# Performance work log

Hardware: AMD Instinct MI355X
Metric: run time of the kernel (lower is better)

## Reference

```python
import jax, jax.numpy as jnp
import numpy as np

B, SEQ, C, H, L = 2, 512, 768, 12, 6
OBS = ACT = GOAL = 64
MAXEP = 1000
D = C // H
T3 = 3 * SEQ  # stacked (z, state, action) tokens per timestep


def _ln(x, g, b):
    m = jnp.mean(x, -1, keepdims=True)
    v = jnp.mean((x - m) ** 2, -1, keepdims=True)
    return (x - m) * jax.lax.rsqrt(v + 1e-5) * g + b


def setup_inputs() -> dict:
    key = jax.random.key(0)
    it = iter(jax.random.split(key, 64))
    nrm = lambda shape, s=0.02: jax.random.normal(next(it), shape, jnp.float32) * s
    z = lambda *s: jnp.zeros(s, jnp.float32)
    o = lambda *s: jnp.ones(s, jnp.float32)
    return dict(
        states=jax.random.normal(next(it), (B, SEQ, OBS), jnp.float32),
        actions=jax.random.normal(next(it), (B, SEQ, ACT), jnp.float32),
        goals=jax.random.normal(next(it), (B, 1, GOAL), jnp.float32),
        traj_mask=jnp.ones((B, SEQ), bool),
        timesteps=jax.random.randint(next(it), (B, SEQ), 0, MAXEP),
        W_s=nrm((OBS, C)), b_s=z(C),
        W_a=nrm((ACT, C)), b_a=z(C),
        W_g=nrm((GOAL, C)), b_g=z(C),
        E_t=nrm((MAXEP, C)),
        ln0_g=o(C), ln0_b=z(C),
        Wq=nrm((L, C, C)), bq=z(L, C),
        Wk=nrm((L, C, C)), bk=z(L, C),
        Wv=nrm((L, C, C)), bv=z(L, C),
        Wp=nrm((L, C, C)), bp=z(L, C),
        ln1_g=o(L, C), ln1_b=z(L, C),
        W1=nrm((L, C, 4 * C)), b1=z(L, 4 * C),
        W2=nrm((L, 4 * C, C)), b2=z(L, C),
        ln2_g=o(L, C), ln2_b=z(L, C),
        W_ps=nrm((C, OBS)), b_ps=z(OBS),
        W_pa=nrm((C, ACT)), b_pa=z(ACT),
    )


def _forward(states, actions, goals, timesteps,
             W_s, b_s, W_a, b_a, W_g, b_g, E_t, ln0_g, ln0_b,
             Wq, bq, Wk, bk, Wv, bv, Wp, bp, ln1_g, ln1_b,
             W1, b1, W2, b2, ln2_g, ln2_b, W_ps, b_ps, W_pa, b_pa):
    te = E_t[timesteps]  # [B,SEQ,C] time embeddings (use_pe_as_timestep path)
    s_emb = states @ W_s + b_s + te
    a_emb = actions @ W_a + b_a + te
    g = jnp.broadcast_to(goals, (goals.shape[0], SEQ, goals.shape[2]))
    z_emb = g @ W_g + b_g + te  # GOAL_CONDITION path
    # interleave (z, s, a) per timestep -> [B, 3*SEQ, C]
    x = jnp.stack((z_emb, s_emb, a_emb), axis=2).reshape(states.shape[0], T3, C)
    x = _ln(x, ln0_g, ln0_b)
    mask = jnp.tril(jnp.ones((T3, T3), bool))
    scale = 1.0 / np.sqrt(D)
    for l in range(L):
        q = (x @ Wq[l] + bq[l]).reshape(-1, T3, H, D)
        k = (x @ Wk[l] + bk[l]).reshape(-1, T3, H, D)
        v = (x @ Wv[l] + bv[l]).reshape(-1, T3, H, D)
        sc = jnp.einsum('bqhd,bkhd->bhqk', q, k) * scale
        sc = jnp.where(mask, sc, -jnp.inf)
        w = jax.nn.softmax(sc, axis=-1)
        att = jnp.einsum('bhqk,bkhd->bqhd', w, v).reshape(-1, T3, C)
        x = x + att @ Wp[l] + bp[l]
        x = _ln(x, ln1_g[l], ln1_b[l])
        h = jax.nn.gelu(x @ W1[l] + b1[l], approximate=False)
        x = x + h @ W2[l] + b2[l]
        x = _ln(x, ln2_g[l], ln2_b[l])
    x = x.reshape(-1, SEQ, 3, C)
    state_preds = x[:, :, 2] @ W_ps + b_ps     # read off action-token positions
    action_preds = jnp.tanh(x[:, :, 1] @ W_pa + b_pa)  # state-token positions
    return jnp.stack((state_preds, action_preds))  # [2,B,SEQ,64]


def reference(states, actions, goals, traj_mask, timesteps,
              W_s, b_s, W_a, b_a, W_g, b_g, E_t, ln0_g, ln0_b,
              Wq, bq, Wk, bk, Wv, bv, Wp, bp, ln1_g, ln1_b,
              W1, b1, W2, b2, ln2_g, ln2_b, W_ps, b_ps, W_pa, b_pa):
    del traj_mask  # unused on the GOAL_CONDITION path
    return _forward(states, actions, goals, timesteps,
                    W_s, b_s, W_a, b_a, W_g, b_g, E_t, ln0_g, ln0_b,
                    Wq, bq, Wk, bk, Wv, bv, Wp, bp, ln1_g, ln1_b,
                    W1, b1, W2, b2, ln2_g, ln2_b, W_ps, b_ps, W_pa, b_pa)
```

## Files before the change

### kernel.cpp

```cpp
#include <hip/hip_runtime.h>

#define SEQ 512
#define T3 1536
#define CDIM 768
#define NH 12
#define HD 64
#define NL 6

typedef __attribute__((ext_vector_type(8))) short bh8;
typedef __attribute__((ext_vector_type(4))) short s4;
typedef __attribute__((ext_vector_type(4))) float f4;

__device__ inline short f2bf(float f) {
    union { float f; unsigned u; } x; x.f = f;
    unsigned r = x.u + 0x7FFFu + ((x.u >> 16) & 1u);
    return (short)(r >> 16);
}

__device__ inline float bf2f(short s) {
    union { unsigned u; float f; } x;
    x.u = ((unsigned)(unsigned short)s) << 16;
    return x.f;
}

__device__ inline void gload16(const short* g, const short* l) {
    __builtin_amdgcn_global_load_lds(
        (const __attribute__((address_space(1))) unsigned int*)g,
        (__attribute__((address_space(3))) unsigned int*)l, 16, 0, 0);
}

__device__ inline float block_sum(float v, volatile float* red, int tid) {
    #pragma unroll
    for (int off = 32; off > 0; off >>= 1) v += __shfl_down(v, off, 64);
    __syncthreads();
    if ((tid & 63) == 0) red[tid >> 6] = v;
    __syncthreads();
    return red[0] + red[1] + red[2] + red[3];
}

__global__ __launch_bounds__(256) void conv64_k(
        const float* __restrict__ Wq, const float* __restrict__ Wk,
        const float* __restrict__ Wv, const float* __restrict__ Wp,
        const float* __restrict__ W1, const float* __restrict__ W2,
        short* __restrict__ dst, int l0) {
    __shared__ float t2[2][64][65];
    int tid = threadIdx.x;
    int rk = tid >> 4, cn4 = (tid & 15) * 4;
    const float* srcA[2]; short* dA[2]; int KA[2], k0A[2], n0A[2];
    f4 vv[2][4];
    #pragma unroll
    for (int i = 0; i < 2; ++i) {
        int tt = blockIdx.x * 2 + i;
        int lrel = tt / 1728, r = tt - lrel * 1728;
        int l = l0 + lrel;
        short* dstL = dst + (size_t)lrel * 7077888;
        const float* src; short* d; int K, N, tk, tn;
        if (r < 576) {
            int mat = r / 144, t = r - mat * 144;
            tk = t / 12; tn = t % 12; K = 768; N = 768;
            const float* srcs[4] = {Wq, Wk, Wv, Wp};
            src = srcs[mat] + (size_t)l * 589824;
            d = dstL + mat * 589824;
        } else if (r < 1152) {
            int t = r - 576; tk = t / 48; tn = t % 48; K = 768; N = 3072;
            src = W1 + (size_t)l * 2359296; d = dstL + 2359296;
        } else {
            int t = r - 1152; tk = t / 12; tn = t % 12; K = 3072; N = 768;
            src = W2 + (size_t)l * 2359296; d = dstL + 4718592;
        }
        int k0 = tk * 64, n0 = tn * 64;
        srcA[i] = src; dA[i] = d; KA[i] = K; k0A[i] = k0; n0A[i] = n0;
        #pragma unroll
        for (int p = 0; p < 4; ++p)
            vv[i][p] = *(const f4*)(src + (size_t)(k0 + p * 16 + rk) * N + n0 + cn4);
    }
    #pragma unroll
    for (int i = 0; i < 2; ++i)
    #pragma unroll
    for (int p = 0; p < 4; ++p) {
        t2[i][cn4][p * 16 + rk]     = vv[i][p][0];
        t2[i][cn4 + 1][p * 16 + rk] = vv[i][p][1];
        t2[i][cn4 + 2][p * 16 + rk] = vv[i][p][2];
        t2[i][cn4 + 3][p * 16 + rk] = vv[i][p][3];
    }
    __syncthreads();
    int n = tid >> 2, kb = (tid & 3) * 16;
    #pragma unroll
    for (int i = 0; i < 2; ++i) {
        f4 a0 = *(const f4*)&t2[i][n][kb];
        f4 a1 = *(const f4*)&t2[i][n][kb + 4];
        f4 a2 = *(const f4*)&t2[i][n][kb + 8];
        f4 a3 = *(const f4*)&t2[i][n][kb + 12];
        bh8 o0, o1;
        o0[0] = f2bf(a0[0]); o0[1] = f2bf(a0[1]); o0[2] = f2bf(a0[2]); o0[3] = f2bf(a0[3]);
        o0[4] = f2bf(a1[0]); o0[5] = f2bf(a1[1]); o0[6] = f2bf(a1[2]); o0[7] = f2bf(a1[3]);
        o1[0] = f2bf(a2[0]); o1[1] = f2bf(a2[1]); o1[2] = f2bf(a2[2]); o1[3] = f2bf(a2[3]);
        o1[4] = f2bf(a3[0]); o1[5] = f2bf(a3[1]); o1[6] = f2bf(a3[2]); o1[7] = f2bf(a3[3]);
        short* wp = dA[i] + (size_t)(n0A[i] + n) * KA[i] + k0A[i] + kb;
        *(bh8*)wp = o0;
        *(bh8*)(wp + 8) = o1;
    }
}

__global__ __launch_bounds__(256) void embed_ln0_k(
        const float* __restrict__ states, const float* __restrict__ actions,
        const float* __restrict__ goals, const int* __restrict__ timesteps,
        const float* __restrict__ W_s, const float* __restrict__ b_s,
        const float* __restrict__ W_a, const float* __restrict__ b_a,
        const float* __restrict__ W_g, const float* __restrict__ b_g,
        const float* __restrict__ E_t, const float* __restrict__ g0,
        const float* __restrict__ bb0, float* __restrict__ x, short* __restrict__ xb) {
    int row = blockIdx.x;
    int b = row / T3, t3 = row - b * T3;
    int t = t3 / 3, kind = t3 - t * 3;
    __shared__ float inv[64];
    __shared__ float xr[CDIM];
    __shared__ float red[4];
    int tid = threadIdx.x;
    const float* src; const float* W; const float* bias;
    if (kind == 0)      { src = goals + b * 64;                       W = W_g; bias = b_g; }
    else if (kind == 1) { src = states + ((size_t)b * SEQ + t) * 64;  W = W_s; bias = b_s; }
    else                { src = actions + ((size_t)b * SEQ + t) * 64; W = W_a; bias = b_a; }
    if (tid < 64) inv[tid] = src[tid];
    __syncthreads();
    int ts = timesteps[b * SEQ + t];
    for (int c = tid; c < CDIM; c += 256) {
        float acc = bias[c] + E_t[(size_t)ts * CDIM + c];
        #pragma unroll 8
        for (int kk = 0; kk < 64; ++kk) acc += inv[kk] * W[kk * CDIM + c];
        xr[c] = acc;
    }
    __syncthreads();
    float v0 = xr[tid], v1 = xr[tid + 256], v2 = xr[tid + 512];
    float mean = block_sum(v0 + v1 + v2, red, tid) * (1.f / CDIM);
    float d0 = v0 - mean, d1 = v1 - mean, d2 = v2 - mean;
    float var = block_sum(d0 * d0 + d1 * d1 + d2 * d2, red, tid) * (1.f / CDIM);
    float rs = rsqrtf(var + 1e-5f);
    float* w = x + (size_t)row * CDIM;
    short* wb = xb + (size_t)row * CDIM;
    float o0 = d0 * rs * g0[tid]       + bb0[tid];
    float o1 = d1 * rs * g0[tid + 256] + bb0[tid + 256];
    float o2 = d2 * rs * g0[tid + 512] + bb0[tid + 512];
    w[tid] = o0; w[tid + 256] = o1; w[tid + 512] = o2;
    wb[tid] = f2bf(o0); wb[tid + 256] = f2bf(o1); wb[tid + 512] = f2bf(o2);
}

__global__ __launch_bounds__(256) void ln_k(float* __restrict__ x, short* __restrict__ outb,
                                            const float* __restrict__ g, const float* __restrict__ bb) {
    int wave = threadIdx.x >> 6, lane = threadIdx.x & 63;
    int row = blockIdx.x * 4 + wave;
    float* r = x + (size_t)row * CDIM;
    short* wb = outb + (size_t)row * CDIM;
    float v[12];
    float s = 0.f, s2 = 0.f;
    #pragma unroll
    for (int j = 0; j < 12; ++j) {
        v[j] = r[lane + j * 64];
        s += v[j]; s2 += v[j] * v[j];
    }
    #pragma unroll
    for (int off = 32; off > 0; off >>= 1) { s += __shfl_xor(s, off, 64); s2 += __shfl_xor(s2, off, 64); }
    float mean = s * (1.f / CDIM);
    float var = s2 * (1.f / CDIM) - mean * mean;
    float rs = rsqrtf(var + 1e-5f);
    #pragma unroll
    for (int j = 0; j < 12; ++j) {
        int c = lane + j * 64;
        float o = (v[j] - mean) * rs * g[c] + bb[c];
        r[c] = o;
        wb[c] = f2bf(o);
    }
}

template<int BM, int BN, int EPI>
__global__ __launch_bounds__(256) void gemm5_k(
        const short* __restrict__ A, const short* __restrict__ B0,
        const short* __restrict__ B1, const short* __restrict__ B2,
        const float* __restrict__ bias0, const float* __restrict__ bias1,
        const float* __restrict__ bias2,
        float* __restrict__ outF, short* __restrict__ outQ,
        short* __restrict__ outK, short* __restrict__ outV,
        int N, int K) {
    const short* Bw = B0; const float* bias = bias0; short* outB = outQ;
    int zid = 0;
    if (EPI == 0) {
        zid = blockIdx.z;
        if (zid == 1) { Bw = B1; bias = bias1; outB = outK; }
        else if (zid == 2) { Bw = B2; bias = bias2; outB = outV; }
    }
    __shared__ short As[BM * 64];
    __shared__ short Bs[BN * 64];
    int tid = threadIdx.x, lane = tid & 63, wave = tid >> 6;
    int wm = wave >> 1, wn = wave & 1, lr = lane & 15, lg = lane >> 4;
    int bm = blockIdx.y * BM, bn = blockIdx.x * BN;
    int rl = lane >> 3, ch = (lane & 7) ^ rl;
    constexpr int MI = BM / 32, NI = BN / 32;
    f4 acc[MI][NI] = {};
    for (int k0 = 0; k0 < K; k0 += 64) {
        #pragma unroll
        for (int j = 0; j < BM / 32; ++j)
            gload16(A + (size_t)(bm + wave * (BM / 4) + j * 8 + rl) * K + k0 + ch * 8,
                    As + (wave * (BM / 4) + j * 8) * 64);
        #pragma unroll
        for (int j = 0; j < BN / 32; ++j)
            gload16(Bw + (size_t)(bn + wave * (BN / 4) + j * 8 + rl) * K + k0 + ch * 8,
                    Bs + (wave * (BN / 4) + j * 8) * 64);
        __syncthreads();
        bh8 af[MI][2], bf[NI][2];
        #pragma unroll
        for (int mi = 0; mi < MI; ++mi)
        #pragma unroll
        for (int kk = 0; kk < 2; ++kk) {
            int m = wm * (BM / 2) + mi * 16 + lr;
            af[mi][kk] = *(const bh8*)(As + m * 64 + (((kk * 4 + lg) ^ (lr & 7)) * 8));
        }
        #pragma unroll
        for (int ni = 0; ni < NI; ++ni)
        #pragma unroll
        for (int kk = 0; kk < 2; ++kk) {
            int n = wn * (BN / 2) + ni * 16 + lr;
            bf[ni][kk] = *(const bh8*)(Bs + n * 64 + (((kk * 4 + lg) ^ (lr & 7)) * 8));
        }
        #pragma unroll
        for (int kk = 0; kk < 2; ++kk)
        #pragma unroll
        for (int mi = 0; mi < MI; ++mi)
        #pragma unroll
        for (int ni = 0; ni < NI; ++ni)
            acc[mi][ni] = __builtin_amdgcn_mfma_f32_16x16x32_bf16(af[mi][kk], bf[ni][kk], acc[mi][ni], 0, 0, 0);
        __syncthreads();
    }
    #pragma unroll
    for (int mi = 0; mi < MI; ++mi)
    #pragma unroll
    for (int ni = 0; ni < NI; ++ni)
    #pragma unroll
    for (int i = 0; i < 4; ++i) {
        int row = bm + wm * (BM / 2) + mi * 16 + lg * 4 + i;
        int col = bn + wn * (BN / 2) + ni * 16 + lr;
        float vv = acc[mi][ni][i] + bias[col];
        if (EPI == 0) {
            int b = row / T3, t = row - b * T3;
            int h = col >> 6, d = col & 63;
            if (zid == 2) outB[((size_t)(b * NH + h) * 64 + d) * T3 + t] = f2bf(vv);
            else          outB[((((size_t)b * NH + h) * T3 + t) << 6) + d] = f2bf(vv);
        } else if (EPI == 1) {
            size_t idx = (size_t)row * N + col;
            outF[idx] = vv + outF[idx];
        } else {
            float gl = 0.5f * vv * (1.0f + erff(vv * 0.70710678118f));
            outQ[(size_t)row * N + col] = f2bf(gl);
        }
    }
}

__global__ __launch_bounds__(256) void attn_k(const short* __restrict__ q, const short* __restrict__ k,
                                              const short* __restrict__ vt, short* __restrict__ att) {
    int idx = blockIdx.x;
    int qt = 23 - (idx / 24);
    int bh = idx % 24;
    int b = bh / NH, h = bh - b * NH;
    const short* qb = q  + (size_t)bh * T3 * HD;
    const short* kb = k  + (size_t)bh * T3 * HD;
    const short* vb = vt + (size_t)bh * HD * T3;
    __shared__ short Ks[2][4096];
    __shared__ short Vs[2][4096];
    __shared__ short Pl[4][16][72];
    int tid = threadIdx.x, lane = tid & 63, wave = tid >> 6;
    int lr = lane & 15, lg = lane >> 4;
    int rl = lane >> 3, ch = (lane & 7) ^ rl;
    int qrow0 = qt * 64 + wave * 16;
    bh8 aq0 = *(const bh8*)(qb + (size_t)(qrow0 + lr) * HD + lg * 8);
    bh8 aq1 = *(const bh8*)(qb + (size_t)(qrow0 + lr) * HD + 32 + lg * 8);
    f4 o[4] = {};
    float lsum[4] = {0.f, 0.f, 0.f, 0.f};

    auto STAGE = [&](int kt2, int buf) {
        const short* kb2 = kb + (size_t)kt2 * 64 * HD;
        #pragma unroll
        for (int j = 0; j < 2; ++j)
            gload16(kb2 + (wave * 16 + j * 8 + rl) * HD + ch * 8,
                    &Ks[buf][(wave * 16 + j * 8) * 64]);
        const short* vb2 = vb + kt2 * 64;
        #pragma unroll
        for (int j = 0; j < 2; ++j)
            gload16(vb2 + (size_t)(wave * 16 + j * 8 + rl) * T3 + ch * 8,
                    &Vs[buf][(wave * 16 + j * 8) * 64]);
    };

    STAGE(0, 0);
    int cur = 0;
    for (int kt = 0; kt <= qt; ++kt) {
        if (kt < qt) {
            STAGE(kt + 1, cur ^ 1);
            asm volatile("s_waitcnt vmcnt(4)" ::: "memory");
        } else {
            asm volatile("s_waitcnt vmcnt(0)" ::: "memory");
        }
        __builtin_amdgcn_s_barrier();
        __builtin_amdgcn_sched_barrier(0);
        const short* Kb = &Ks[cur][0];
        const short* Vb = &Vs[cur][0];
        f4 s[4];
        #pragma unroll
        for (int nf = 0; nf < 4; ++nf) {
            int tok = nf * 16 + lr;
            bh8 bk0 = *(const bh8*)(Kb + tok * 64 + ((lg ^ (lr & 7)) * 8));
            bh8 bk1 = *(const bh8*)(Kb + tok * 64 + (((4 + lg) ^ (lr & 7)) * 8));
            f4 t = {};
            t = __builtin_amdgcn_mfma_f32_16x16x32_bf16(aq0, bk0, t, 0, 0, 0);
            t = __builtin_amdgcn_mfma_f32_16x16x32_bf16(aq1, bk1, t, 0, 0, 0);
            s[nf] = t;
        }
        #pragma unroll
        for (int nf = 0; nf < 4; ++nf)
        #pragma unroll
        for (int i = 0; i < 4; ++i) {
            float p = __expf(s[nf][i] * 0.125f);
            if (kt == qt && (nf * 16 + lr) > (wave * 16 + lg * 4 + i)) p = 0.f;
            lsum[i] += p;
            Pl[wave][lg * 4 + i][nf * 16 + lr] = f2bf(p);
        }
        bh8 ap0 = *(const bh8*)&Pl[wave][lr][lg * 8];
        bh8 ap1 = *(const bh8*)&Pl[wave][lr][32 + lg * 8];
        #pragma unroll
        for (int nf = 0; nf < 4; ++nf) {
            int d = nf * 16 + lr;
            bh8 bv0 = *(const bh8*)(Vb + d * 64 + ((lg ^ (lr & 7)) * 8));
            bh8 bv1 = *(const bh8*)(Vb + d * 64 + (((4 + lg) ^ (lr & 7)) * 8));
            o[nf] = __builtin_amdgcn_mfma_f32_16x16x32_bf16(ap0, bv0, o[nf], 0, 0, 0);
            o[nf] = __builtin_amdgcn_mfma_f32_16x16x32_bf16(ap1, bv1, o[nf], 0, 0, 0);
        }
        __builtin_amdgcn_sched_barrier(0);
        __builtin_amdgcn_s_barrier();
        cur ^= 1;
    }
    float linv[4];
    #pragma unroll
    for (int i = 0; i < 4; ++i) {
        float l = lsum[i];
        #pragma unroll
        for (int off = 1; off < 16; off <<= 1) l += __shfl_xor(l, off, 16);
        linv[i] = 1.f / l;
    }
    #pragma unroll
    for (int nf = 0; nf < 4; ++nf)
    #pragma unroll
    for (int i = 0; i < 4; ++i) {
        int qrow = qrow0 + lg * 4 + i;
        att[((size_t)b * T3 + qrow) * CDIM + h * 64 + nf * 16 + lr] = f2bf(o[nf][i] * linv[i]);
    }
}

__global__ __launch_bounds__(64) void head_k(const short* __restrict__ x,
                                             const float* __restrict__ Wps, const float* __restrict__ bps,
                                             const float* __restrict__ Wpa, const float* __restrict__ bpa,
                                             float* __restrict__ out) {
    int o = blockIdx.y;
    int bs = blockIdx.x;
    int b = bs >> 9, t = bs & 511;
    int kind = (o == 0) ? 2 : 1;
    const float* W = (o == 0) ? Wps : Wpa;
    const float* bi = (o == 0) ? bps : bpa;
    const short* xr = x + ((size_t)b * T3 + t * 3 + kind) * CDIM;
    int n = threadIdx.x;
    float a0 = 0.f, a1 = 0.f, a2 = 0.f, a3 = 0.f;
    for (int kk = 0; kk < CDIM; kk += 4) {
        s4 xv = *(const s4*)(xr + kk);
        a0 = fmaf(bf2f(xv[0]), W[(kk)     * 64 + n], a0);
        a1 = fmaf(bf2f(xv[1]), W[(kk + 1) * 64 + n], a1);
        a2 = fmaf(bf2f(xv[2]), W[(kk + 2) * 64 + n], a2);
        a3 = fmaf(bf2f(xv[3]), W[(kk + 3) * 64 + n], a3);
    }
    float acc = bi[n] + ((a0 + a1) + (a2 + a3));
    if (o == 1) acc = tanhf(acc);
    out[(((size_t)o * 2 + b) * SEQ + t) * 64 + n] = acc;
}

extern "C" void kernel_launch(void* const* d_in, const int* in_sizes, int n_in,
                              void* d_out, int out_size, void* d_ws, size_t ws_size,
                              hipStream_t stream) {
    const float* states    = (const float*)d_in[0];
    const float* actions   = (const float*)d_in[1];
    const float* goals     = (const float*)d_in[2];
    const int*   timesteps = (const int*)d_in[4];
    const float* W_s = (const float*)d_in[5];  const float* b_s = (const float*)d_in[6];
    const float* W_a = (const float*)d_in[7];  const float* b_a = (const float*)d_in[8];
    const float* W_g = (const float*)d_in[9];  const float* b_g = (const float*)d_in[10];
    const float* E_t = (const float*)d_in[11];
    const float* ln0_g = (const float*)d_in[12]; const float* ln0_b = (const float*)d_in[13];
    const float* Wq = (const float*)d_in[14]; const float* bq = (const float*)d_in[15];
    const float* Wk = (const float*)d_in[16]; const float* bk = (const float*)d_in[17];
    const float* Wv = (const float*)d_in[18]; const float* bv = (const float*)d_in[19];
    const float* Wp = (const float*)d_in[20]; const float* bp = (const float*)d_in[21];
    const float* ln1_g = (const float*)d_in[22]; const float* ln1_b = (const float*)d_in[23];
    const float* W1 = (const float*)d_in[24]; const float* b1 = (const float*)d_in[25];
    const float* W2 = (const float*)d_in[26]; const float* b2 = (const float*)d_in[27];
    const float* ln2_g = (const float*)d_in[28]; const float* ln2_b = (const float*)d_in[29];
    const float* W_ps = (const float*)d_in[30]; const float* b_ps = (const float*)d_in[31];
    const float* W_pa = (const float*)d_in[32]; const float* b_pa = (const float*)d_in[33];

    char* ws = (char*)d_ws;
    float* x_f   = (float*)(ws);
    short* x_bf  = (short*)(ws + 9437184);
    short* h_bf  = (short*)(ws + 14155776);
    short* qb    = (short*)(ws + 14155776);
    short* kb    = (short*)(ws + 18874368);
    short* vbt   = (short*)(ws + 23592960);
    short* wts   = (short*)(ws + 33030144);

    const long long WL = 7077888;
    bool allw = ws_size >= 117964800ull;

    embed_ln0_k<<<dim3(2 * T3), 256, 0, stream>>>(states, actions, goals, timesteps,
        W_s, b_s, W_a, b_a, W_g, b_g, E_t, ln0_g, ln0_b, x_f, x_bf);

    if (allw)
        conv64_k<<<dim3(1728 * NL / 2), 256, 0, stream>>>(Wq, Wk, Wv, Wp, W1, W2, wts, 0);

    for (int l = 0; l < NL; ++l) {
        size_t bo = (size_t)l * CDIM, b1o = (size_t)l * 4 * CDIM;
        if (!allw)
            conv64_k<<<dim3(1728 / 2), 256, 0, stream>>>(Wq, Wk, Wv, Wp, W1, W2, wts, l);
        short* wb  = wts + (allw ? (long long)l * WL : 0);
        short* Wqt = wb;
        short* Wkt = wb + 589824;
        short* Wvt = wb + 1179648;
        short* Wpt = wb + 1769472;
        short* W1t = wb + 2359296;
        short* W2t = wb + 4718592;

        gemm5_k<64, 64, 0><<<dim3(12, 48, 3), 256, 0, stream>>>(x_bf, Wqt, Wkt, Wvt,
            bq + bo, bk + bo, bv + bo, nullptr, qb, kb, vbt, CDIM, CDIM);
        attn_k<<<dim3(576), 256, 0, stream>>>(qb, kb, vbt, x_bf);
        gemm5_k<64, 64, 1><<<dim3(12, 48, 1), 256, 0, stream>>>(x_bf, Wpt, nullptr, nullptr,
            bp + bo, nullptr, nullptr, x_f, nullptr, nullptr, nullptr, CDIM, CDIM);
        ln_k<<<dim3(768), 256, 0, stream>>>(x_f, x_bf, ln1_g + bo, ln1_b + bo);
        gemm5_k<128, 64, 2><<<dim3(48, 24, 1), 256, 0, stream>>>(x_bf, W1t, nullptr, nullptr,
            b1 + b1o, nullptr, nullptr, nullptr, h_bf, nullptr, nullptr, 4 * CDIM, CDIM);
        gemm5_k<64, 64, 1><<<dim3(12, 48, 1), 256, 0, stream>>>(h_bf, W2t, nullptr, nullptr,
            b2 + bo, nullptr, nullptr, x_f, nullptr, nullptr, nullptr, CDIM, 4 * CDIM);
        ln_k<<<dim3(768), 256, 0, stream>>>(x_f, x_bf, ln2_g + bo, ln2_b + bo);
    }

    head_k<<<dim3(1024, 2), 64, 0, stream>>>(x_bf, W_ps, b_ps, W_pa, b_pa, (float*)d_out);
}
```

Measured before the change: 1.083 ms.

## Enlarge attention query tile to 128 rows and QKV GEMM M-tile

The attention kernel now gives each wave 32 query rows (two 16-row MFMA tiles) and each block a 128-row query tile, so every staged K/V tile in shared memory is reused across twice as many queries. This halves the number of attention blocks (288) and the total K/V global traffic, at the cost of more registers per wave and less parallelism. Causal masking is generalized to the two diagonal key tiles per query tile. The QKV projection GEMM also switches to a 128-row tile with half as many row blocks.

```diff
diff --git a/kernel.cpp b/kernel.cpp
--- a/kernel.cpp
+++ b/kernel.cpp
@@ -257,7 +257,7 @@
 __global__ __launch_bounds__(256) void attn_k(const short* __restrict__ q, const short* __restrict__ k,
                                               const short* __restrict__ vt, short* __restrict__ att) {
     int idx = blockIdx.x;
-    int qt = 23 - (idx / 24);
+    int qt = 11 - (idx / 24);
     int bh = idx % 24;
     int b = bh / NH, h = bh - b * NH;
     const short* qb = q  + (size_t)bh * T3 * HD;
@@ -265,15 +265,19 @@
     const short* vb = vt + (size_t)bh * HD * T3;
     __shared__ short Ks[2][4096];
     __shared__ short Vs[2][4096];
-    __shared__ short Pl[4][16][72];
+    __shared__ short Pl[4][32][72];
     int tid = threadIdx.x, lane = tid & 63, wave = tid >> 6;
     int lr = lane & 15, lg = lane >> 4;
     int rl = lane >> 3, ch = (lane & 7) ^ rl;
-    int qrow0 = qt * 64 + wave * 16;
-    bh8 aq0 = *(const bh8*)(qb + (size_t)(qrow0 + lr) * HD + lg * 8);
-    bh8 aq1 = *(const bh8*)(qb + (size_t)(qrow0 + lr) * HD + 32 + lg * 8);
-    f4 o[4] = {};
-    float lsum[4] = {0.f, 0.f, 0.f, 0.f};
+    int qw0 = qt * 128 + wave * 32;
+    bh8 aq[2][2];
+    #pragma unroll
+    for (int mi = 0; mi < 2; ++mi) {
+        aq[mi][0] = *(const bh8*)(qb + (size_t)(qw0 + mi * 16 + lr) * HD + lg * 8);
+        aq[mi][1] = *(const bh8*)(qb + (size_t)(qw0 + mi * 16 + lr) * HD + 32 + lg * 8);
+    }
+    f4 o[2][4] = {};
+    float lsum[2][4] = {};
 
     auto STAGE = [&](int kt2, int buf) {
         const short* kb2 = kb + (size_t)kt2 * 64 * HD;
@@ -288,10 +292,11 @@
                     &Vs[buf][(wave * 16 + j * 8) * 64]);
     };
 
+    int nkt = 2 * qt + 2;
     STAGE(0, 0);
     int cur = 0;
-    for (int kt = 0; kt <= qt; ++kt) {
-        if (kt < qt) {
+    for (int kt = 0; kt < nkt; ++kt) {
+        if (kt + 1 < nkt) {
             STAGE(kt + 1, cur ^ 1);
             asm volatile("s_waitcnt vmcnt(4)" ::: "memory");
         } else {
@@ -301,54 +306,70 @@
         __builtin_amdgcn_sched_barrier(0);
         const short* Kb = &Ks[cur][0];
         const short* Vb = &Vs[cur][0];
-        f4 s[4];
+        f4 s[2][4];
         #pragma unroll
         for (int nf = 0; nf < 4; ++nf) {
             int tok = nf * 16 + lr;
             bh8 bk0 = *(const bh8*)(Kb + tok * 64 + ((lg ^ (lr & 7)) * 8));
             bh8 bk1 = *(const bh8*)(Kb + tok * 64 + (((4 + lg) ^ (lr & 7)) * 8));
-            f4 t = {};
-            t = __builtin_amdgcn_mfma_f32_16x16x32_bf16(aq0, bk0, t, 0, 0, 0);
-            t = __builtin_amdgcn_mfma_f32_16x16x32_bf16(aq1, bk1, t, 0, 0, 0);
-            s[nf] = t;
-        }
+            #pragma unroll
+            for (int mi = 0; mi < 2; ++mi) {
+                f4 t = {};
+                t = __builtin_amdgcn_mfma_f32_16x16x32_bf16(aq[mi][0], bk0, t, 0, 0, 0);
+                t = __builtin_amdgcn_mfma_f32_16x16x32_bf16(aq[mi][1], bk1, t, 0, 0, 0);
+                s[mi][nf] = t;
+            }
+        }
+        bool diag = (kt >= 2 * qt);
+        #pragma unroll
+        for (int mi = 0; mi < 2; ++mi)
         #pragma unroll
         for (int nf = 0; nf < 4; ++nf)
         #pragma unroll
         for (int i = 0; i < 4; ++i) {
-            float p = __expf(s[nf][i] * 0.125f);
-            if (kt == qt && (nf * 16 + lr) > (wave * 16 + lg * 4 + i)) p = 0.f;
-            lsum[i] += p;
-            Pl[wave][lg * 4 + i][nf * 16 + lr] = f2bf(p);
-        }
-        bh8 ap0 = *(const bh8*)&Pl[wave][lr][lg * 8];
-        bh8 ap1 = *(const bh8*)&Pl[wave][lr][32 + lg * 8];
+            float p = __expf(s[mi][nf][i] * 0.125f);
+            if (diag && (kt * 64 + nf * 16 + lr) > (qw0 + mi * 16 + lg * 4 + i)) p = 0.f;
+            lsum[mi][i] += p;
+            Pl[wave][mi * 16 + lg * 4 + i][nf * 16 + lr] = f2bf(p);
+        }
+        bh8 ap[2][2];
+        #pragma unroll
+        for (int mi = 0; mi < 2; ++mi) {
+            ap[mi][0] = *(const bh8*)&Pl[wave][mi * 16 + lr][lg * 8];
+            ap[mi][1] = *(const bh8*)&Pl[wave][mi * 16 + lr][32 + lg * 8];
+        }
         #pragma unroll
         for (int nf = 0; nf < 4; ++nf) {
             int d = nf * 16 + lr;
             bh8 bv0 = *(const bh8*)(Vb + d * 64 + ((lg ^ (lr & 7)) * 8));
             bh8 bv1 = *(const bh8*)(Vb + d * 64 + (((4 + lg) ^ (lr & 7)) * 8));
-            o[nf] = __builtin_amdgcn_mfma_f32_16x16x32_bf16(ap0, bv0, o[nf], 0, 0, 0);
-            o[nf] = __builtin_amdgcn_mfma_f32_16x16x32_bf16(ap1, bv1, o[nf], 0, 0, 0);
+            #pragma unroll
+            for (int mi = 0; mi < 2; ++mi) {
+                o[mi][nf] = __builtin_amdgcn_mfma_f32_16x16x32_bf16(ap[mi][0], bv0, o[mi][nf], 0, 0, 0);
+                o[mi][nf] = __builtin_amdgcn_mfma_f32_16x16x32_bf16(ap[mi][1], bv1, o[mi][nf], 0, 0, 0);
+            }
         }
         __builtin_amdgcn_sched_barrier(0);
         __builtin_amdgcn_s_barrier();
         cur ^= 1;
     }
-    float linv[4];
-    #pragma unroll
-    for (int i = 0; i < 4; ++i) {
-        float l = lsum[i];
-        #pragma unroll
-        for (int off = 1; off < 16; off <<= 1) l += __shfl_xor(l, off, 16);
-        linv[i] = 1.f / l;
-    }
-    #pragma unroll
-    for (int nf = 0; nf < 4; ++nf)
-    #pragma unroll
-    for (int i = 0; i < 4; ++i) {
-        int qrow = qrow0 + lg * 4 + i;
-        att[((size_t)b * T3 + qrow) * CDIM + h * 64 + nf * 16 + lr] = f2bf(o[nf][i] * linv[i]);
+    #pragma unroll
+    for (int mi = 0; mi < 2; ++mi) {
+        float linv[4];
+        #pragma unroll
+        for (int i = 0; i < 4; ++i) {
+            float l = lsum[mi][i];
+            #pragma unroll
+            for (int off = 1; off < 16; off <<= 1) l += __shfl_xor(l, off, 16);
+            linv[i] = 1.f / l;
+        }
+        #pragma unroll
+        for (int nf = 0; nf < 4; ++nf)
+        #pragma unroll
+        for (int i = 0; i < 4; ++i) {
+            int qrow = qw0 + mi * 16 + lg * 4 + i;
+            att[((size_t)b * T3 + qrow) * CDIM + h * 64 + nf * 16 + lr] = f2bf(o[mi][nf][i] * linv[i]);
+        }
     }
 }
 
@@ -430,9 +451,9 @@
         short* W1t = wb + 2359296;
         short* W2t = wb + 4718592;
 
-        gemm5_k<64, 64, 0><<<dim3(12, 48, 3), 256, 0, stream>>>(x_bf, Wqt, Wkt, Wvt,
+        gemm5_k<128, 64, 0><<<dim3(12, 24, 3), 256, 0, stream>>>(x_bf, Wqt, Wkt, Wvt,
             bq + bo, bk + bo, bv + bo, nullptr, qb, kb, vbt, CDIM, CDIM);
-        attn_k<<<dim3(576), 256, 0, stream>>>(qb, kb, vbt, x_bf);
+        attn_k<<<dim3(288), 256, 0, stream>>>(qb, kb, vbt, x_bf);
         gemm5_k<64, 64, 1><<<dim3(12, 48, 1), 256, 0, stream>>>(x_bf, Wpt, nullptr, nullptr,
             bp + bo, nullptr, nullptr, x_f, nullptr, nullptr, nullptr, CDIM, CDIM);
         ln_k<<<dim3(768), 256, 0, stream>>>(x_f, x_bf, ln1_g + bo, ln1_b + bo);
```

New measurement: 1.212 ms. 1.12x slower.
